# Kernel tuning notes

Hardware: AMD Instinct MI355X
Metric: run time of the kernel (lower is better)

Reference implementation:

```python
import jax, jax.numpy as jnp
import numpy as np

N = 100000   # nodes
E = 3200000  # directed edges
F_IN = 128   # data.num_node_features
H = 16       # hidden
C = 2        # output classes (hard-coded in module)


def _glorot(key, fan_in, fan_out):
    s = jnp.sqrt(6.0 / (fan_in + fan_out)).astype(jnp.float32)
    return jax.random.uniform(key, (fan_in, fan_out), jnp.float32, -s, s)


def setup_inputs() -> dict:
    key = jax.random.key(0)
    ks = jax.random.split(key, 5)
    x = jax.random.normal(ks[0], (N, F_IN), jnp.float32)
    edge_index = jax.random.randint(ks[1], (2, E), 0, N, dtype=jnp.int64)
    return {
        "x": x,
        "edge_index": edge_index,
        "W1": _glorot(ks[2], F_IN, H), "b1": jnp.zeros((H,), jnp.float32),
        "W2": _glorot(ks[3], H, H),    "b2": jnp.zeros((H,), jnp.float32),
        "W3": _glorot(ks[4], H, C),    "b3": jnp.zeros((C,), jnp.float32),
    }


def _gcn_conv(x, W, b, src, dst, norm, n):
    # PyG GCNConv: linear transform, then normalized gather -> scatter-add, + bias
    h = x @ W                                   # [N, out]
    msg = h[src] * norm[:, None]                # [E+N, out] gather over source nodes
    out = jax.ops.segment_sum(msg, dst, num_segments=n)  # scatter-add at targets
    return out + b


def reference(x, edge_index, W1, b1, W2, b2, W3, b3):
    n = x.shape[0]
    loop = jnp.arange(n, dtype=edge_index.dtype)
    src = jnp.concatenate([edge_index[0], loop])  # add self-loops (PyG default)
    dst = jnp.concatenate([edge_index[1], loop])
    # symmetric normalization: deg^{-1/2}[src] * deg^{-1/2}[dst], deg = in-degree w/ self-loops
    deg = jax.ops.segment_sum(jnp.ones(src.shape, jnp.float32), dst, num_segments=n)
    dis = jnp.where(deg > 0, jax.lax.rsqrt(jnp.maximum(deg, 1.0)), 0.0)
    norm = dis[src] * dis[dst]
    # dropout is identity in eval mode
    h = jax.nn.relu(_gcn_conv(x, W1, b1, src, dst, norm, n))
    h = jax.nn.relu(_gcn_conv(h, W2, b2, src, dst, norm, n))
    h = _gcn_conv(h, W3, b3, src, dst, norm, n)
    return jax.nn.log_softmax(h, axis=1)
```

## Files before the change

kernel.cpp:

```cpp
#include <hip/hip_runtime.h>
#include <math.h>

#define NSB  1024
#define BSH  9
#define BKN  512
#define TPB  8

typedef _Float16 h8  __attribute__((ext_vector_type(8)));
typedef _Float16 h2v __attribute__((ext_vector_type(2)));


__global__ void k_scan1(const int* __restrict__ in, int* __restrict__ out,
                        int* __restrict__ bsum, int n) {
    __shared__ int sd[256];
    int base = blockIdx.x * 2048 + threadIdx.x * 8;
    int v[8];
    int ts = 0;
#pragma unroll
    for (int j = 0; j < 8; j++) {
        int idx = base + j;
        v[j] = ts;
        ts += (idx < n) ? in[idx] : 0;
    }
    sd[threadIdx.x] = ts;
    __syncthreads();
    for (int ofs = 1; ofs < 256; ofs <<= 1) {
        int t = (threadIdx.x >= (unsigned)ofs) ? sd[threadIdx.x - ofs] : 0;
        __syncthreads();
        sd[threadIdx.x] += t;
        __syncthreads();
    }
    int excl = (threadIdx.x == 0) ? 0 : sd[threadIdx.x - 1];
#pragma unroll
    for (int j = 0; j < 8; j++) {
        int idx = base + j;
        if (idx < n) out[idx] = excl + v[j];
    }
    if (threadIdx.x == 255) bsum[blockIdx.x] = sd[255];
}

__global__ void k_scan2(int* __restrict__ bsum, int nb) {
    __shared__ int sd[256];
    int orig = (threadIdx.x < (unsigned)nb) ? bsum[threadIdx.x] : 0;
    sd[threadIdx.x] = orig;
    __syncthreads();
    for (int ofs = 1; ofs < 256; ofs <<= 1) {
        int t = (threadIdx.x >= (unsigned)ofs) ? sd[threadIdx.x - ofs] : 0;
        __syncthreads();
        sd[threadIdx.x] += t;
        __syncthreads();
    }
    if (threadIdx.x < (unsigned)nb) bsum[threadIdx.x] = sd[threadIdx.x] - orig;
}

__global__ void k_scan3(int* __restrict__ out, const int* __restrict__ bsum, int n) {
    int i = blockIdx.x * blockDim.x + threadIdx.x;
    if (i < n) out[i] += bsum[i >> 11];
}


__global__ void k_hist(const int* __restrict__ dst, int* __restrict__ hist,
                       int e, int nbuck, int es) {
    __shared__ int h[256];
    for (int i = threadIdx.x; i < 256; i += blockDim.x) h[i] = 0;
    __syncthreads();
    int lo = blockIdx.x * es;
    int hi = min(lo + es, e);
    for (int i = lo + threadIdx.x; i < hi; i += blockDim.x)
        atomicAdd(&h[dst[i] >> BSH], 1);
    __syncthreads();
    for (int i = threadIdx.x; i < nbuck; i += blockDim.x)
        hist[(size_t)i * gridDim.x + blockIdx.x] = h[i];
}

__global__ void k_bucket(const int* __restrict__ src, const int* __restrict__ dst,
                         const int* __restrict__ offs, unsigned* __restrict__ col,
                         int e, int nbuck, int es) {
    __shared__ int cur[256];
    for (int i = threadIdx.x; i < nbuck; i += blockDim.x)
        cur[i] = offs[(size_t)i * gridDim.x + blockIdx.x];
    __syncthreads();
    int lo = blockIdx.x * es;
    int hi = min(lo + es, e);
    for (int i = lo + threadIdx.x; i < hi; i += blockDim.x) {
        int d = dst[i];
        int b = d >> BSH;
        int pos = atomicAdd(&cur[b], 1);
        col[pos] = ((unsigned)src[i] << BSH) | (unsigned)(d & (BKN - 1));
    }
}

__global__ void k_sort(const unsigned* __restrict__ col, const int* __restrict__ offs,
                       int* __restrict__ col2, int* __restrict__ rs,
                       float* __restrict__ dis, int n, int e, int nbuck) {
    __shared__ int cnt[BKN];
    __shared__ int sd[BKN];
    __shared__ int cur[BKN];
    int tid = threadIdx.x;
    int b = blockIdx.x;
    int lo = offs[(size_t)b * NSB];
    int hi = (b + 1 < nbuck) ? offs[(size_t)(b + 1) * NSB] : e;
    if (tid < BKN) cnt[tid] = 0;
    __syncthreads();
    for (int i = lo + tid; i < hi; i += 1024)
        atomicAdd(&cnt[col[i] & (BKN - 1u)], 1);
    __syncthreads();
    if (tid < BKN) sd[tid] = cnt[tid];
    __syncthreads();
    for (int ofs = 1; ofs < BKN; ofs <<= 1) {
        int t = (tid < BKN && tid >= ofs) ? sd[tid - ofs] : 0;
        __syncthreads();
        if (tid < BKN) sd[tid] += t;
        __syncthreads();
    }
    if (tid < BKN) {
        int excl = (tid == 0) ? 0 : sd[tid - 1];
        cur[tid] = lo + excl;
        int node = (b << BSH) + tid;
        if (node < n) {
            rs[node] = lo + excl;
            dis[node] = rsqrtf((float)(cnt[tid] + 1));
        }
    }
    if (b == 0 && tid == 0) rs[n] = e;
    __syncthreads();
    for (int i = lo + tid; i < hi; i += 1024) {
        unsigned v = col[i];
        int pos = atomicAdd(&cur[v & (BKN - 1u)], 1);
        col2[pos] = (int)(v >> BSH);
    }
}


__global__ void k_linear1s(const float* __restrict__ x, const float* __restrict__ W,
                           const float* __restrict__ dis, _Float16* __restrict__ hs,
                           int n, int ntiles) {
    __shared__ float sWT[16 * 132];
    __shared__ float sx[16 * 132];
    int tid = threadIdx.x;
    for (int i = tid; i < 2048; i += 256) {
        int k = i >> 4, c = i & 15;
        sWT[c * 132 + k] = W[i];
    }
    int tile0 = blockIdx.x * TPB;
    const float4* xg4 = (const float4*)x;
    for (int tile = tile0; tile < tile0 + TPB && tile < ntiles; tile++) {
        int nodeBase = tile * 16;
        __syncthreads();
        for (int i = tid; i < 512; i += 256) {
            int nl = i >> 5, k4 = i & 31;
            int nd = nodeBase + nl;
            float4 v = make_float4(0.f, 0.f, 0.f, 0.f);
            if (nd < n) v = xg4[(size_t)nd * 32 + k4];
            *((float4*)(sx + nl * 132 + k4 * 4)) = v;
        }
        __syncthreads();
        int nl = tid >> 4, c = tid & 15;
        int node = nodeBase + nl;
        const float4* xr = (const float4*)(sx + nl * 132);
        const float4* wr = (const float4*)(sWT + c * 132);
        float acc = 0.f;
#pragma unroll
        for (int k4 = 0; k4 < 32; k4++) {
            float4 xv = xr[k4];
            float4 wv = wr[k4];
            acc += xv.x * wv.x + xv.y * wv.y + xv.z * wv.z + xv.w * wv.w;
        }
        if (node < n)
            hs[(size_t)node * 16 + c] = (_Float16)(acc * dis[node]);
    }
}


__global__ void k_pullA(const _Float16* __restrict__ hs, const int* __restrict__ rs,
                        const int* __restrict__ col2, const float* __restrict__ dis,
                        const float* __restrict__ bb, const float* __restrict__ W,
                        _Float16* __restrict__ hsOut, int n) {
    __shared__ float sW[256];
    __shared__ float sb[16];
    if (threadIdx.x < 256) sW[threadIdx.x] = W[threadIdx.x];
    if (threadIdx.x < 16) sb[threadIdx.x] = bb[threadIdx.x];
    __syncthreads();
    int t = blockIdx.x * blockDim.x + threadIdx.x;
    int node = t >> 1, q = t & 1;
    if (node >= n) return;
    const h8* H = (const h8*)hs;
    h8 self = H[(size_t)node * 2 + q];
    float acc[8];
#pragma unroll
    for (int j = 0; j < 8; j++) acc[j] = (float)self[j];
    int b = rs[node], e2 = rs[node + 1];
    int i = b;
    for (; i + 3 < e2; i += 4) {
        int s0 = col2[i], s1 = col2[i + 1], s2 = col2[i + 2], s3 = col2[i + 3];
        h8 v0 = H[(size_t)s0 * 2 + q];
        h8 v1 = H[(size_t)s1 * 2 + q];
        h8 v2 = H[(size_t)s2 * 2 + q];
        h8 v3 = H[(size_t)s3 * 2 + q];
#pragma unroll
        for (int j = 0; j < 8; j++)
            acc[j] += (float)v0[j] + (float)v1[j] + (float)v2[j] + (float)v3[j];
    }
    for (; i < e2; i++) {
        h8 v = H[(size_t)col2[i] * 2 + q];
#pragma unroll
        for (int j = 0; j < 8; j++) acc[j] += (float)v[j];
    }
    float d = dis[node];
    float va[16];
#pragma unroll
    for (int j = 0; j < 8; j++) {
        int k = q * 8 + j;
        float v = acc[j] * d + sb[k];
        v = v > 0.f ? v : 0.f;
        float other = __shfl_xor(v, 1);
        va[j]     = q ? other : v;
        va[8 + j] = q ? v : other;
    }
    h8 o;
#pragma unroll
    for (int j = 0; j < 8; j++) {
        int c = q * 8 + j;
        float s = 0.f;
#pragma unroll
        for (int k = 0; k < 16; k++) s += va[k] * sW[k * 16 + c];
        o[j] = (_Float16)(s * d);
    }
    ((h8*)hsOut)[(size_t)node * 2 + q] = o;
}


__global__ void k_pullB(const _Float16* __restrict__ hs, const int* __restrict__ rs,
                        const int* __restrict__ col2, const float* __restrict__ dis,
                        const float* __restrict__ bb, const float* __restrict__ W,
                        _Float16* __restrict__ hs2, int n) {
    __shared__ float sW[32];
    __shared__ float sb[16];
    if (threadIdx.x < 32) sW[threadIdx.x] = W[threadIdx.x];
    if (threadIdx.x < 16) sb[threadIdx.x] = bb[threadIdx.x];
    __syncthreads();
    int t = blockIdx.x * blockDim.x + threadIdx.x;
    int node = t >> 1, q = t & 1;
    if (node >= n) return;
    const h8* H = (const h8*)hs;
    h8 self = H[(size_t)node * 2 + q];
    float acc[8];
#pragma unroll
    for (int j = 0; j < 8; j++) acc[j] = (float)self[j];
    int b = rs[node], e2 = rs[node + 1];
    int i = b;
    for (; i + 3 < e2; i += 4) {
        int s0 = col2[i], s1 = col2[i + 1], s2 = col2[i + 2], s3 = col2[i + 3];
        h8 v0 = H[(size_t)s0 * 2 + q];
        h8 v1 = H[(size_t)s1 * 2 + q];
        h8 v2 = H[(size_t)s2 * 2 + q];
        h8 v3 = H[(size_t)s3 * 2 + q];
#pragma unroll
        for (int j = 0; j < 8; j++)
            acc[j] += (float)v0[j] + (float)v1[j] + (float)v2[j] + (float)v3[j];
    }
    for (; i < e2; i++) {
        h8 v = H[(size_t)col2[i] * 2 + q];
#pragma unroll
        for (int j = 0; j < 8; j++) acc[j] += (float)v[j];
    }
    float d = dis[node];
    float p0 = 0.f, p1 = 0.f;
#pragma unroll
    for (int j = 0; j < 8; j++) {
        int k = q * 8 + j;
        float v = acc[j] * d + sb[k];
        v = v > 0.f ? v : 0.f;
        p0 += v * sW[k * 2 + 0];
        p1 += v * sW[k * 2 + 1];
    }
    p0 += __shfl_xor(p0, 1);
    p1 += __shfl_xor(p1, 1);
    if (q == 0) {
        h2v o;
        o[0] = (_Float16)(p0 * d);
        o[1] = (_Float16)(p1 * d);
        ((h2v*)hs2)[node] = o;
    }
}


__global__ void k_pull2lsm(const _Float16* __restrict__ hs2, const int* __restrict__ rs,
                           const int* __restrict__ col2, const float* __restrict__ dis,
                           const float* __restrict__ b3, float* __restrict__ out, int n) {
    int node = blockIdx.x * blockDim.x + threadIdx.x;
    if (node >= n) return;
    const h2v* H = (const h2v*)hs2;
    h2v self = H[node];
    float a0 = (float)self[0], a1 = (float)self[1];
    int b = rs[node], e2 = rs[node + 1];
    int i = b;
    for (; i + 3 < e2; i += 4) {
        h2v v0 = H[col2[i]];
        h2v v1 = H[col2[i + 1]];
        h2v v2 = H[col2[i + 2]];
        h2v v3 = H[col2[i + 3]];
        a0 += (float)v0[0] + (float)v1[0] + (float)v2[0] + (float)v3[0];
        a1 += (float)v0[1] + (float)v1[1] + (float)v2[1] + (float)v3[1];
    }
    for (; i < e2; i++) {
        h2v v = H[col2[i]];
        a0 += (float)v[0];
        a1 += (float)v[1];
    }
    float d = dis[node];
    float z0 = a0 * d + b3[0];
    float z1 = a1 * d + b3[1];
    float m = fmaxf(z0, z1);
    float l = m + logf(expf(z0 - m) + expf(z1 - m));
    float2 o = {z0 - l, z1 - l};
    ((float2*)out)[node] = o;
}


extern "C" void kernel_launch(void* const* d_in, const int* in_sizes, int n_in,
                              void* d_out, int out_size, void* d_ws, size_t ws_size,
                              hipStream_t stream) {
    const float* x  = (const float*)d_in[0];
    const int*   ei = (const int*)d_in[1];
    const float* W1 = (const float*)d_in[2];
    const float* b1 = (const float*)d_in[3];
    const float* W2 = (const float*)d_in[4];
    const float* b2 = (const float*)d_in[5];
    const float* W3 = (const float*)d_in[6];
    const float* b3 = (const float*)d_in[7];
    float* out = (float*)d_out;

    const int N = in_sizes[0] / 128;
    const int E = in_sizes[1] / 2;
    const int* src = ei;
    const int* dst = ei + E;

    const int NBUCK = (N + BKN - 1) >> BSH;
    const int M = NBUCK * NSB;
    const int ES = (E + NSB - 1) / NSB;

    char* ws = (char*)d_ws;
    size_t off = 0;
    auto alloc = [&](size_t bytes) {
        void* p = ws + off;
        off += (bytes + 255) & ~(size_t)255;
        return p;
    };
    int*       hist = (int*)alloc((size_t)M * sizeof(int));
    int*       offs = (int*)alloc((size_t)M * sizeof(int));
    int*       bsum = (int*)alloc(256 * sizeof(int));
    unsigned*  col  = (unsigned*)alloc((size_t)E * sizeof(unsigned));
    int*       col2 = (int*)alloc((size_t)E * sizeof(int));
    int*       rs   = (int*)alloc((size_t)(N + 1) * sizeof(int));
    float*     dis  = (float*)alloc((size_t)N * sizeof(float));
    _Float16*  hsA  = (_Float16*)alloc((size_t)N * 16 * sizeof(_Float16));
    _Float16*  hsB  = (_Float16*)alloc((size_t)N * 16 * sizeof(_Float16));
    _Float16*  hs2  = (_Float16*)alloc((size_t)N * 2 * sizeof(_Float16));

    const int B = 256;
    auto g = [&](long long work) { return (int)((work + B - 1) / B); };
    const int NBS = (M + 2047) / 2048;

    k_hist<<<NSB, B, 0, stream>>>(dst, hist, E, NBUCK, ES);
    k_scan1<<<NBS, 256, 0, stream>>>(hist, offs, bsum, M);
    k_scan2<<<1, 256, 0, stream>>>(bsum, NBS);
    k_scan3<<<g(M), B, 0, stream>>>(offs, bsum, M);
    k_bucket<<<NSB, B, 0, stream>>>(src, dst, offs, col, E, NBUCK, ES);
    k_sort<<<NBUCK, 1024, 0, stream>>>(col, offs, col2, rs, dis, N, E, NBUCK);

    const int NTILES = (N + 15) / 16;
    k_linear1s<<<(NTILES + TPB - 1) / TPB, B, 0, stream>>>(x, W1, dis, hsA, N, NTILES);

    k_pullA<<<g((long long)N * 2), B, 0, stream>>>(hsA, rs, col2, dis, b1, W2, hsB, N);

    k_pullB<<<g((long long)N * 2), B, 0, stream>>>(hsB, rs, col2, dis, b2, W3, hs2, N);

    k_pull2lsm<<<g(N), B, 0, stream>>>(hs2, rs, col2, dis, b3, out, N);
}
```

Baseline: 283.5 us.

## Stage bucket scatter through shared memory for coalesced global writes

```diff
diff --git a/kernel.cpp b/kernel.cpp
--- a/kernel.cpp
+++ b/kernel.cpp
@@ -1,9 +1,10 @@
 #include <hip/hip_runtime.h>
 #include <math.h>
 
-#define NSB  1024
+#define NSB  512
 #define BSH  9
 #define BKN  512
+#define ESMAX 6272
 #define TPB  8
 
 typedef _Float16 h8  __attribute__((ext_vector_type(8)));
@@ -76,17 +77,42 @@
 __global__ void k_bucket(const int* __restrict__ src, const int* __restrict__ dst,
                          const int* __restrict__ offs, unsigned* __restrict__ col,
                          int e, int nbuck, int es) {
-    __shared__ int cur[256];
-    for (int i = threadIdx.x; i < nbuck; i += blockDim.x)
-        cur[i] = offs[(size_t)i * gridDim.x + blockIdx.x];
+    __shared__ unsigned sorted[ESMAX];
+    __shared__ unsigned char sbuck[ESMAX];
+    __shared__ int lc[256], lsc[256], lofE[256], lcur[256], soff[256];
+    int tid = threadIdx.x;
+    lc[tid] = 0;
+    if (tid < nbuck) soff[tid] = offs[(size_t)tid * gridDim.x + blockIdx.x];
     __syncthreads();
     int lo = blockIdx.x * es;
     int hi = min(lo + es, e);
-    for (int i = lo + threadIdx.x; i < hi; i += blockDim.x) {
+    for (int i = lo + tid; i < hi; i += 256)
+        atomicAdd(&lc[dst[i] >> BSH], 1);
+    __syncthreads();
+    lsc[tid] = lc[tid];
+    __syncthreads();
+    for (int ofs = 1; ofs < 256; ofs <<= 1) {
+        int t = (tid >= ofs) ? lsc[tid - ofs] : 0;
+        __syncthreads();
+        lsc[tid] += t;
+        __syncthreads();
+    }
+    int excl = (tid == 0) ? 0 : lsc[tid - 1];
+    lofE[tid] = excl;
+    lcur[tid] = excl;
+    __syncthreads();
+    for (int i = lo + tid; i < hi; i += 256) {
         int d = dst[i];
         int b = d >> BSH;
-        int pos = atomicAdd(&cur[b], 1);
-        col[pos] = ((unsigned)src[i] << BSH) | (unsigned)(d & (BKN - 1));
+        int p = atomicAdd(&lcur[b], 1);
+        sorted[p] = ((unsigned)src[i] << BSH) | (unsigned)(d & (BKN - 1));
+        sbuck[p] = (unsigned char)b;
+    }
+    __syncthreads();
+    int cnt = hi - lo;
+    for (int i = tid; i < cnt; i += 256) {
+        int b = sbuck[i];
+        col[soff[b] + (i - lofE[b])] = sorted[i];
     }
 }
 
```

After: 281.4 us. No clear change (-0.7%).
